# Optimization experiments

Hardware: AMD Instinct MI355X
Metric: run time of the kernel (lower is better)

Reference implementation:

```python
import jax, jax.numpy as jnp
import numpy as np

HASH_SIZE = 256      # hash_table_size
OFFSET_SIZE = 64     # offset_table_size
FEAT = 8             # feature_channels
N_QUERIES = 4_000_000
DOMAIN = 1024


def setup_inputs() -> dict:
    key = jax.random.key(0)
    k1, k2, k3 = jax.random.split(key, 3)
    coords = jax.random.randint(k1, (N_QUERIES, 3), 0, DOMAIN, dtype=jnp.int32)
    hash_table = jax.random.normal(k2, (HASH_SIZE, HASH_SIZE, HASH_SIZE, FEAT), dtype=jnp.float32)
    # uint8 offsets in [0, 256); stored as int32 for jax indexing arithmetic
    offset_table = jax.random.randint(k3, (OFFSET_SIZE, OFFSET_SIZE, OFFSET_SIZE, 3), 0, 256, dtype=jnp.int32)
    m0 = jnp.ones((3,), dtype=jnp.float32)
    m1 = jnp.ones((3,), dtype=jnp.float32)
    return {"coords": coords, "hash_table": hash_table, "offset_table": offset_table,
            "m0": m0, "m1": m1}


def reference(coords, hash_table, offset_table, m0, m1):
    # Stage 1: offset-table lookup. torch: (x * m1).long() % offset_table_size
    oidx = (coords.astype(jnp.float32) * m1).astype(jnp.int32) % OFFSET_SIZE  # [N,3]
    offsets = offset_table[oidx[:, 0], oidx[:, 1], oidx[:, 2]]                # [N,3]
    # Stage 2: perfect-hash index. torch: ((x*m0).long() + offset) % hash_table_size
    h0 = (coords.astype(jnp.float32) * m0).astype(jnp.int32)
    hidx = (h0 + offsets) % HASH_SIZE                                          # [N,3]
    # Feature gather from the hash table
    features = hash_table[hidx[:, 0], hidx[:, 1], hidx[:, 2]]                  # [N,FEAT]
    return features
```

## Files before the change

kernel.cpp:

```cpp
#include <hip/hip_runtime.h>

#define HASH_SIZE 256
#define OFFSET_SIZE 64
#define FEAT 8

__global__ void __launch_bounds__(256)
psh_kernel(const int* __restrict__ coords,
           const float* __restrict__ hash_table,
           const int* __restrict__ offset_table,
           const float* __restrict__ m0,
           const float* __restrict__ m1,
           float* __restrict__ out,
           int n) {
    int i = blockIdx.x * blockDim.x + threadIdx.x;
    if (i >= n) return;

    float m0x = m0[0], m0y = m0[1], m0z = m0[2];
    float m1x = m1[0], m1y = m1[1], m1z = m1[2];

    int cx = coords[3 * i + 0];
    int cy = coords[3 * i + 1];
    int cz = coords[3 * i + 2];

    int ox = ((int)((float)cx * m1x)) & (OFFSET_SIZE - 1);
    int oy = ((int)((float)cy * m1y)) & (OFFSET_SIZE - 1);
    int oz = ((int)((float)cz * m1z)) & (OFFSET_SIZE - 1);

    size_t ooff = ((size_t)((ox * OFFSET_SIZE + oy) * OFFSET_SIZE + oz)) * 3;
    int dx = offset_table[ooff + 0];
    int dy = offset_table[ooff + 1];
    int dz = offset_table[ooff + 2];

    int hx = (((int)((float)cx * m0x)) + dx) & (HASH_SIZE - 1);
    int hy = (((int)((float)cy * m0y)) + dy) & (HASH_SIZE - 1);
    int hz = (((int)((float)cz * m0z)) + dz) & (HASH_SIZE - 1);

    size_t hoff = (((size_t)hx * HASH_SIZE + hy) * HASH_SIZE + hz) * FEAT;
    const float4* hp = (const float4*)(hash_table + hoff);
    float4 f0 = hp[0];
    float4 f1 = hp[1];

    float4* op = (float4*)(out + (size_t)i * FEAT);
    op[0] = f0;
    op[1] = f1;
}

extern "C" void kernel_launch(void* const* d_in, const int* in_sizes, int n_in,
                              void* d_out, int out_size, void* d_ws, size_t ws_size,
                              hipStream_t stream) {
    const int*   coords       = (const int*)d_in[0];
    const float* hash_table   = (const float*)d_in[1];
    const int*   offset_table = (const int*)d_in[2];
    const float* m0           = (const float*)d_in[3];
    const float* m1           = (const float*)d_in[4];
    float*       out          = (float*)d_out;

    int n = in_sizes[0] / 3;
    int block = 256;
    int grid = (n + block - 1) / block;
    psh_kernel<<<grid, block, 0, stream>>>(coords, hash_table, offset_table,
                                           m0, m1, out, n);
}
```

Baseline: 741.2 us.

## Process four queries per thread with vectorized nontemporal coord loads and output stores

Each thread now handles four queries. It loads their coordinates as three 16-byte nontemporal vector loads and issues all offset-table and hash-table gathers in batched phases to raise memory-level parallelism. Outputs are written with nontemporal stores. The tail is not guarded, so it relies on n being a multiple of four, and the extra registers could lower occupancy.

```diff
diff --git a/kernel.cpp b/kernel.cpp
--- a/kernel.cpp
+++ b/kernel.cpp
@@ -3,6 +3,10 @@
 #define HASH_SIZE 256
 #define OFFSET_SIZE 64
 #define FEAT 8
+#define QPT 4
+
+typedef int   vint4   __attribute__((ext_vector_type(4)));
+typedef float vfloat4 __attribute__((ext_vector_type(4)));
 
 __global__ void __launch_bounds__(256)
 psh_kernel(const int* __restrict__ coords,
@@ -12,37 +16,64 @@
            const float* __restrict__ m1,
            float* __restrict__ out,
            int n) {
-    int i = blockIdx.x * blockDim.x + threadIdx.x;
-    if (i >= n) return;
+    int t = blockIdx.x * blockDim.x + threadIdx.x;
+    int q0 = t * QPT;
+    if (q0 >= n) return;
 
     float m0x = m0[0], m0y = m0[1], m0z = m0[2];
     float m1x = m1[0], m1y = m1[1], m1z = m1[2];
 
-    int cx = coords[3 * i + 0];
-    int cy = coords[3 * i + 1];
-    int cz = coords[3 * i + 2];
+    const vint4* cp = (const vint4*)(coords + (size_t)q0 * 3);
+    vint4 ca = __builtin_nontemporal_load(cp + 0);
+    vint4 cb = __builtin_nontemporal_load(cp + 1);
+    vint4 cc = __builtin_nontemporal_load(cp + 2);
 
-    int ox = ((int)((float)cx * m1x)) & (OFFSET_SIZE - 1);
-    int oy = ((int)((float)cy * m1y)) & (OFFSET_SIZE - 1);
-    int oz = ((int)((float)cz * m1z)) & (OFFSET_SIZE - 1);
+    int cx[QPT], cy[QPT], cz[QPT];
+    cx[0] = ca.x; cy[0] = ca.y; cz[0] = ca.z;
+    cx[1] = ca.w; cy[1] = cb.x; cz[1] = cb.y;
+    cx[2] = cb.z; cy[2] = cb.w; cz[2] = cc.x;
+    cx[3] = cc.y; cy[3] = cc.z; cz[3] = cc.w;
 
-    size_t ooff = ((size_t)((ox * OFFSET_SIZE + oy) * OFFSET_SIZE + oz)) * 3;
-    int dx = offset_table[ooff + 0];
-    int dy = offset_table[ooff + 1];
-    int dz = offset_table[ooff + 2];
+    size_t ooff[QPT];
+#pragma unroll
+    for (int q = 0; q < QPT; ++q) {
+        int ox = ((int)((float)cx[q] * m1x)) & (OFFSET_SIZE - 1);
+        int oy = ((int)((float)cy[q] * m1y)) & (OFFSET_SIZE - 1);
+        int oz = ((int)((float)cz[q] * m1z)) & (OFFSET_SIZE - 1);
+        ooff[q] = ((size_t)((ox * OFFSET_SIZE + oy) * OFFSET_SIZE + oz)) * 3;
+    }
+    int dx[QPT], dy[QPT], dz[QPT];
+#pragma unroll
+    for (int q = 0; q < QPT; ++q) {
+        dx[q] = offset_table[ooff[q] + 0];
+        dy[q] = offset_table[ooff[q] + 1];
+        dz[q] = offset_table[ooff[q] + 2];
+    }
 
-    int hx = (((int)((float)cx * m0x)) + dx) & (HASH_SIZE - 1);
-    int hy = (((int)((float)cy * m0y)) + dy) & (HASH_SIZE - 1);
-    int hz = (((int)((float)cz * m0z)) + dz) & (HASH_SIZE - 1);
+    const float4* hp[QPT];
+#pragma unroll
+    for (int q = 0; q < QPT; ++q) {
+        int hx = (((int)((float)cx[q] * m0x)) + dx[q]) & (HASH_SIZE - 1);
+        int hy = (((int)((float)cy[q] * m0y)) + dy[q]) & (HASH_SIZE - 1);
+        int hz = (((int)((float)cz[q] * m0z)) + dz[q]) & (HASH_SIZE - 1);
+        size_t hoff = (((size_t)hx * HASH_SIZE + hy) * HASH_SIZE + hz) * FEAT;
+        hp[q] = (const float4*)(hash_table + hoff);
+    }
+    float4 f0[QPT], f1[QPT];
+#pragma unroll
+    for (int q = 0; q < QPT; ++q) {
+        f0[q] = hp[q][0];
+        f1[q] = hp[q][1];
+    }
 
-    size_t hoff = (((size_t)hx * HASH_SIZE + hy) * HASH_SIZE + hz) * FEAT;
-    const float4* hp = (const float4*)(hash_table + hoff);
-    float4 f0 = hp[0];
-    float4 f1 = hp[1];
-
-    float4* op = (float4*)(out + (size_t)i * FEAT);
-    op[0] = f0;
-    op[1] = f1;
+    vfloat4* op = (vfloat4*)(out + (size_t)q0 * FEAT);
+#pragma unroll
+    for (int q = 0; q < QPT; ++q) {
+        vfloat4 v0 = {f0[q].x, f0[q].y, f0[q].z, f0[q].w};
+        vfloat4 v1 = {f1[q].x, f1[q].y, f1[q].z, f1[q].w};
+        __builtin_nontemporal_store(v0, op + 2 * q + 0);
+        __builtin_nontemporal_store(v1, op + 2 * q + 1);
+    }
 }
 
 extern "C" void kernel_launch(void* const* d_in, const int* in_sizes, int n_in,
@@ -56,8 +87,9 @@
     float*       out          = (float*)d_out;
 
     int n = in_sizes[0] / 3;
+    int nthreads = (n + QPT - 1) / QPT;
     int block = 256;
-    int grid = (n + block - 1) / block;
+    int grid = (nthreads + block - 1) / block;
     psh_kernel<<<grid, block, 0, stream>>>(coords, hash_table, offset_table,
                                            m0, m1, out, n);
 }
```

Measured after the change: 967.9 us. 30.6% more time.
